# Optimization experiments

Measured on AMD Instinct MI355X. Metric: run time of the kernel, lower is better.

## Reference

```python
import jax, jax.numpy as jnp
import numpy as np


def setup_inputs() -> dict:
    key = jax.random.key(0)
    k1, k2, k3 = jax.random.split(key, 3)
    B, N, c = 8, 4096, 512
    heads, K, head_dim = 16, 1024, 64
    X = jax.random.normal(k1, (B, N, c), dtype=jnp.float32)
    ind = jax.random.randint(k2, (B, heads, K), 0, N, dtype=jnp.int64)
    bound = 1.0 / np.sqrt(head_dim)
    W = jax.random.uniform(k3, (heads, c, head_dim), dtype=jnp.float32,
                           minval=-bound, maxval=bound)
    return {"X": X, "ind": ind, "W": W}


def reference(X, ind, W):
    # X: (B, N, c); ind: (B, heads, K); W: (heads, c, head_dim)
    # Gather tokens per head: (B, heads, K, c)
    X_gathered = jnp.take_along_axis(
        X[:, None, :, :],                  # (B, 1, N, c)
        ind[..., None],                    # (B, heads, K, 1)
        axis=2,
    )
    # Per-head projection: (B, heads, K, head_dim)
    out = jnp.einsum('beki,eij->bekj', X_gathered, W)
    return out
```

## Files before the change

kernel.cpp:

```cpp
#include <hip/hip_runtime.h>

typedef __attribute__((ext_vector_type(8))) short short8;
typedef __attribute__((ext_vector_type(16))) float f32x16;

#define B_    8
#define N_TOK 4096
#define C_    512
#define H_    16
#define K_TOK 1024
#define D_    64
#define BM    64
#define BK    64

static __device__ inline ushort f2b(float f) {
  unsigned u = __builtin_bit_cast(unsigned, f);
  u += 0x7fff + ((u >> 16) & 1);
  return (ushort)(u >> 16);
}

__global__ __launch_bounds__(256) void wt_convert(const float* __restrict__ W,
                                                  ushort* __restrict__ WT) {
  __shared__ float tile[64][65];
  int h   = blockIdx.x >> 3;
  int kc0 = (blockIdx.x & 7) << 6;
  int t   = threadIdx.x;
  const float* Wh = W + ((size_t)h * C_ + kc0) * D_;
#pragma unroll
  for (int p = 0; p < 4; ++p) {
    int k  = p * 16 + (t >> 4);
    int n4 = (t & 15) * 4;
    float4 v = *reinterpret_cast<const float4*>(&Wh[k * D_ + n4]);
    tile[k][n4 + 0] = v.x; tile[k][n4 + 1] = v.y;
    tile[k][n4 + 2] = v.z; tile[k][n4 + 3] = v.w;
  }
  __syncthreads();
  ushort* WTh = WT + (size_t)h * D_ * C_;
#pragma unroll
  for (int p = 0; p < 4; ++p) {
    int n  = p * 16 + (t >> 4);
    int k4 = (t & 15) * 4;
    ushort4 o;
    o.x = f2b(tile[k4 + 0][n]); o.y = f2b(tile[k4 + 1][n]);
    o.z = f2b(tile[k4 + 2][n]); o.w = f2b(tile[k4 + 3][n]);
    *reinterpret_cast<ushort4*>(&WTh[n * C_ + kc0 + k4]) = o;
  }
}

__global__ __launch_bounds__(256) void gather_gemm(
    const float* __restrict__ X, const int* __restrict__ ind,
    const ushort* __restrict__ WT, float* __restrict__ out) {
  __shared__ ushort Asu[BM * BK];
  __shared__ ushort Bsu[D_ * BK];
  __shared__ int inds[BM];

  int bid = blockIdx.x;
  int nb = (bid & 7) * 256 + (bid >> 3);
  int b  = nb >> 8;
  int h  = (nb >> 4) & 15;
  int mt = nb & 15;

  int tid = threadIdx.x;
  if (tid < BM) inds[tid] = ind[(size_t)(b * H_ + h) * K_TOK + mt * BM + tid];
  __syncthreads();

  int lane = tid & 63;
  int wave = tid >> 6;
  int r16  = tid >> 4;
  int c4   = tid & 15;

  f32x16 acc = {};

  const float*  Xb  = X + (size_t)b * N_TOK * C_;
  const ushort* wth = WT + (size_t)(h * D_) * C_;

  int rh = wave >> 1;
  int ch = wave & 1;
  int arow = rh * 32 + (lane & 31);
  int brow = ch * 32 + (lane & 31);
  int hi   = lane >> 5;

  int aoff[4];
#pragma unroll
  for (int rr = 0; rr < 4; ++rr)
    aoff[rr] = inds[rr * 16 + r16] * C_ + c4 * 4;
  int boff[2];
#pragma unroll
  for (int t2 = 0; t2 < 2; ++t2) {
    int lin = tid + 256 * t2;
    boff[t2] = (lin >> 3) * C_ + (lin & 7) * 8;
  }

  for (int kc = 0; kc < C_ / BK; ++kc) {
    if (kc) __syncthreads();

    float4 av[4];
#pragma unroll
    for (int rr = 0; rr < 4; ++rr)
      av[rr] = *reinterpret_cast<const float4*>(&Xb[aoff[rr] + kc * BK]);
    uint4 bv[2];
#pragma unroll
    for (int t2 = 0; t2 < 2; ++t2)
      bv[t2] = *reinterpret_cast<const uint4*>(&wth[boff[t2] + kc * BK]);

#pragma unroll
    for (int rr = 0; rr < 4; ++rr) {
      int row = rr * 16 + r16;
      ushort4 w;
      w.x = f2b(av[rr].x); w.y = f2b(av[rr].y);
      w.z = f2b(av[rr].z); w.w = f2b(av[rr].w);
      int sw = (c4 >> 1) ^ (row & 7);
      *reinterpret_cast<ushort4*>(&Asu[row * 64 + sw * 8 + (c4 & 1) * 4]) = w;
    }
#pragma unroll
    for (int t2 = 0; t2 < 2; ++t2) {
      int lin = tid + 256 * t2;
      int n  = lin >> 3;
      int cc = lin & 7;
      *reinterpret_cast<uint4*>(&Bsu[n * 64 + ((cc ^ (n & 7)) << 3)]) = bv[t2];
    }
    __syncthreads();

#pragma unroll
    for (int kk = 0; kk < 4; ++kk) {
      int ka = kk * 2 + hi;
      short8 af = *reinterpret_cast<short8*>(
          &Asu[arow * 64 + ((ka ^ (arow & 7)) << 3)]);
      short8 bf = *reinterpret_cast<short8*>(
          &Bsu[brow * 64 + ((ka ^ (brow & 7)) << 3)]);
      acc = __builtin_amdgcn_mfma_f32_32x32x16_bf16(af, bf, acc, 0, 0, 0);
    }
  }

  size_t obase = ((size_t)(b * H_ + h) * K_TOK + mt * BM + rh * 32) * D_;
  int col = ch * 32 + (lane & 31);
#pragma unroll
  for (int reg = 0; reg < 16; ++reg) {
    int r = (reg & 3) + 8 * (reg >> 2) + 4 * hi;
    out[obase + (size_t)r * D_ + col] = acc[reg];
  }
}

extern "C" void kernel_launch(void* const* d_in, const int* in_sizes, int n_in,
                              void* d_out, int out_size, void* d_ws, size_t ws_size,
                              hipStream_t stream) {
  const float* X  = (const float*)d_in[0];
  const int*  ind = (const int*)d_in[1];
  const float* W  = (const float*)d_in[2];
  float* out = (float*)d_out;
  ushort* WT = (ushort*)d_ws;

  wt_convert<<<dim3(128), dim3(256), 0, stream>>>(W, WT);
  gather_gemm<<<dim3(2048), dim3(256), 0, stream>>>(X, ind, WT, out);
}
```

Baseline: 128.0 us.

## Pre-convert X to bf16 and double-buffer direct global-to-LDS loads

Adds a separate pass that converts the whole X tensor to bf16 in the workspace. The gather-GEMM then fetches rows with global_load_lds straight into swizzled LDS tiles, double-buffered so the next K chunk loads while MFMAs run on the current one. The aim is to halve the bytes fetched per gathered row, remove per-tile fp32-to-bf16 conversion and register staging, and overlap loads with compute. In exchange it adds a full-tensor conversion pass and doubles the LDS footprint.

```diff
diff --git a/kernel.cpp b/kernel.cpp
--- a/kernel.cpp
+++ b/kernel.cpp
@@ -16,6 +16,23 @@
   unsigned u = __builtin_bit_cast(unsigned, f);
   u += 0x7fff + ((u >> 16) & 1);
   return (ushort)(u >> 16);
+}
+
+static __device__ inline void gload_lds16(const ushort* g, ushort* l) {
+  __builtin_amdgcn_global_load_lds(
+      (const __attribute__((address_space(1))) unsigned int*)g,
+      (__attribute__((address_space(3))) unsigned int*)l, 16, 0, 0);
+}
+
+__global__ __launch_bounds__(256) void x_convert(const float* __restrict__ X,
+                                                 ushort* __restrict__ Xb) {
+  size_t base = ((size_t)blockIdx.x * 256 + threadIdx.x) * 8;
+  float4 a = *reinterpret_cast<const float4*>(&X[base]);
+  float4 b = *reinterpret_cast<const float4*>(&X[base + 4]);
+  short8 o;
+  o[0] = f2b(a.x); o[1] = f2b(a.y); o[2] = f2b(a.z); o[3] = f2b(a.w);
+  o[4] = f2b(b.x); o[5] = f2b(b.y); o[6] = f2b(b.z); o[7] = f2b(b.w);
+  *reinterpret_cast<short8*>(&Xb[base]) = o;
 }
 
 __global__ __launch_bounds__(256) void wt_convert(const float* __restrict__ W,
@@ -47,10 +64,10 @@
 }
 
 __global__ __launch_bounds__(256) void gather_gemm(
-    const float* __restrict__ X, const int* __restrict__ ind,
+    const ushort* __restrict__ Xbf, const int* __restrict__ ind,
     const ushort* __restrict__ WT, float* __restrict__ out) {
-  __shared__ ushort Asu[BM * BK];
-  __shared__ ushort Bsu[D_ * BK];
+  __shared__ ushort As[2][BM * BK];
+  __shared__ ushort Bs[2][D_ * BK];
   __shared__ int inds[BM];
 
   int bid = blockIdx.x;
@@ -64,71 +81,53 @@
   __syncthreads();
 
   int lane = tid & 63;
-  int wave = tid >> 6;
-  int r16  = tid >> 4;
-  int c4   = tid & 15;
+  int w    = tid >> 6;
+
+  int rA0 = w * 16 + (lane >> 3);
+  int rA1 = rA0 + 8;
+  int cA  = lane & 7;
+  const ushort* Xb = Xbf + (size_t)b * N_TOK * C_;
+  const ushort* wth = WT + (size_t)(h * D_) * C_;
+  const ushort* gA0 = Xb + (size_t)inds[rA0] * C_ + ((cA ^ (rA0 & 7)) << 3);
+  const ushort* gA1 = Xb + (size_t)inds[rA1] * C_ + ((cA ^ (rA1 & 7)) << 3);
+  const ushort* gB0 = wth + rA0 * C_ + ((cA ^ (rA0 & 7)) << 3);
+  const ushort* gB1 = wth + rA1 * C_ + ((cA ^ (rA1 & 7)) << 3);
+  int lb0 = (w * 16) * 64;
+  int lb1 = lb0 + 8 * 64;
 
   f32x16 acc = {};
-
-  const float*  Xb  = X + (size_t)b * N_TOK * C_;
-  const ushort* wth = WT + (size_t)(h * D_) * C_;
-
-  int rh = wave >> 1;
-  int ch = wave & 1;
+  int rh = w >> 1;
+  int ch = w & 1;
   int arow = rh * 32 + (lane & 31);
   int brow = ch * 32 + (lane & 31);
   int hi   = lane >> 5;
 
-  int aoff[4];
-#pragma unroll
-  for (int rr = 0; rr < 4; ++rr)
-    aoff[rr] = inds[rr * 16 + r16] * C_ + c4 * 4;
-  int boff[2];
-#pragma unroll
-  for (int t2 = 0; t2 < 2; ++t2) {
-    int lin = tid + 256 * t2;
-    boff[t2] = (lin >> 3) * C_ + (lin & 7) * 8;
-  }
+  gload_lds16(gA0, &As[0][lb0]);
+  gload_lds16(gA1, &As[0][lb1]);
+  gload_lds16(gB0, &Bs[0][lb0]);
+  gload_lds16(gB1, &Bs[0][lb1]);
+  __syncthreads();
 
+  int buf = 0;
   for (int kc = 0; kc < C_ / BK; ++kc) {
-    if (kc) __syncthreads();
-
-    float4 av[4];
-#pragma unroll
-    for (int rr = 0; rr < 4; ++rr)
-      av[rr] = *reinterpret_cast<const float4*>(&Xb[aoff[rr] + kc * BK]);
-    uint4 bv[2];
-#pragma unroll
-    for (int t2 = 0; t2 < 2; ++t2)
-      bv[t2] = *reinterpret_cast<const uint4*>(&wth[boff[t2] + kc * BK]);
-
-#pragma unroll
-    for (int rr = 0; rr < 4; ++rr) {
-      int row = rr * 16 + r16;
-      ushort4 w;
-      w.x = f2b(av[rr].x); w.y = f2b(av[rr].y);
-      w.z = f2b(av[rr].z); w.w = f2b(av[rr].w);
-      int sw = (c4 >> 1) ^ (row & 7);
-      *reinterpret_cast<ushort4*>(&Asu[row * 64 + sw * 8 + (c4 & 1) * 4]) = w;
+    if (kc < C_ / BK - 1) {
+      int o = (kc + 1) * BK;
+      gload_lds16(gA0 + o, &As[buf ^ 1][lb0]);
+      gload_lds16(gA1 + o, &As[buf ^ 1][lb1]);
+      gload_lds16(gB0 + o, &Bs[buf ^ 1][lb0]);
+      gload_lds16(gB1 + o, &Bs[buf ^ 1][lb1]);
     }
-#pragma unroll
-    for (int t2 = 0; t2 < 2; ++t2) {
-      int lin = tid + 256 * t2;
-      int n  = lin >> 3;
-      int cc = lin & 7;
-      *reinterpret_cast<uint4*>(&Bsu[n * 64 + ((cc ^ (n & 7)) << 3)]) = bv[t2];
-    }
-    __syncthreads();
-
 #pragma unroll
     for (int kk = 0; kk < 4; ++kk) {
       int ka = kk * 2 + hi;
       short8 af = *reinterpret_cast<short8*>(
-          &Asu[arow * 64 + ((ka ^ (arow & 7)) << 3)]);
+          &As[buf][arow * 64 + ((ka ^ (arow & 7)) << 3)]);
       short8 bf = *reinterpret_cast<short8*>(
-          &Bsu[brow * 64 + ((ka ^ (brow & 7)) << 3)]);
+          &Bs[buf][brow * 64 + ((ka ^ (brow & 7)) << 3)]);
       acc = __builtin_amdgcn_mfma_f32_32x32x16_bf16(af, bf, acc, 0, 0, 0);
     }
+    __syncthreads();
+    buf ^= 1;
   }
 
   size_t obase = ((size_t)(b * H_ + h) * K_TOK + mt * BM + rh * 32) * D_;
@@ -147,8 +146,11 @@
   const int*  ind = (const int*)d_in[1];
   const float* W  = (const float*)d_in[2];
   float* out = (float*)d_out;
-  ushort* WT = (ushort*)d_ws;
+  ushort* WS  = (ushort*)d_ws;
+  ushort* WT  = WS;
+  ushort* Xbf = WS + (size_t)H_ * D_ * C_;
 
+  x_convert<<<dim3(8192), dim3(256), 0, stream>>>(X, Xbf);
   wt_convert<<<dim3(128), dim3(256), 0, stream>>>(W, WT);
-  gather_gemm<<<dim3(2048), dim3(256), 0, stream>>>(X, ind, WT, out);
+  gather_gemm<<<dim3(2048), dim3(256), 0, stream>>>(Xbf, ind, WT, out);
 }
```

After: 129.4 us. About the same (+1.1%).
